# Kernel optimization log

Hardware: AMD Instinct MI355X
Metric: run time of the kernel (lower is better)

## Reference

```python
import jax, jax.numpy as jnp
import numpy as np

DIM = 768
NUM_HEADS = 8
SCALE = (DIM // NUM_HEADS) ** -0.5  # 96^-0.5, matches head_dim**-0.5
B, N = 8, 4096


def setup_inputs() -> dict:
    key = jax.random.key(0)
    k1, k2 = jax.random.split(key)
    x_1 = jax.random.normal(k1, (B, N, DIM), dtype=jnp.float32)
    x_2 = jax.random.normal(k2, (B, N, DIM), dtype=jnp.float32)
    return {"x_1": x_1, "x_2": x_2}


def reference(x_1, x_2):
    # q = x_1, k = v = x_2; channel-wise (transpose) attention
    # attn[b,c,d] = sum_n q[b,n,c] * k[b,n,d] * scale   -> [B, C, C]
    attn = jnp.einsum('bnc,bnd->bcd', x_1, x_2) * SCALE
    attn = jax.nn.softmax(attn, axis=-1)
    # out[b,c,n] = sum_d attn[b,c,d] * v[b,n,d]          -> [B, C, N]
    return jnp.einsum('bcd,bnd->bcn', attn, x_2)
```

## Files before the change

### kernel.cpp

```cpp
#include <hip/hip_runtime.h>
#include <stdint.h>

typedef _Float16 f16;
typedef _Float16 f16x4 __attribute__((ext_vector_type(4)));
typedef _Float16 f16x8 __attribute__((ext_vector_type(8)));
typedef float f32x4 __attribute__((ext_vector_type(4)));

#define NB 8
#define NN 4096
#define CC 768
#define SCALE_F 0.10206207261596577f

#define GLDS16(gp, lp)                                                       \
  __builtin_amdgcn_global_load_lds(                                          \
      (__attribute__((address_space(1))) void*)(gp),                         \
      (__attribute__((address_space(3))) void*)(lp), 16, 0, 0)

__global__ __launch_bounds__(256) void k_convert(
    const float* __restrict__ x1, const float* __restrict__ x2,
    f16* __restrict__ x1t, f16* __restrict__ x2t, f16* __restrict__ x2b) {
  __shared__ float tile[64][65];
  const int which = blockIdx.z >> 3;
  const int b = blockIdx.z & 7;
  const int n0 = blockIdx.x << 6;
  const int c0 = blockIdx.y << 6;
  const float* src = (which ? x2 : x1) + (size_t)b * NN * CC;
  f16* dt = (which ? x2t : x1t) + (size_t)b * CC * NN;
  const int t = threadIdx.x;
  const int rowi = t >> 4;
  const int col4 = (t & 15) << 2;
#pragma unroll
  for (int it = 0; it < 4; ++it) {
    const int r = it * 16 + rowi;
    const float4 v =
        *reinterpret_cast<const float4*>(&src[(size_t)(n0 + r) * CC + c0 + col4]);
    tile[r][col4 + 0] = v.x;
    tile[r][col4 + 1] = v.y;
    tile[r][col4 + 2] = v.z;
    tile[r][col4 + 3] = v.w;
    if (which) {
      f16x4 o = {(f16)v.x, (f16)v.y, (f16)v.z, (f16)v.w};
      *reinterpret_cast<f16x4*>(
          &x2b[(size_t)b * NN * CC + (size_t)(n0 + r) * CC + c0 + col4]) = o;
    }
  }
  __syncthreads();
  const int c = t >> 2;
  const int nb = (t & 3) << 4;
  f16x8 lo, hi;
#pragma unroll
  for (int j = 0; j < 8; ++j) lo[j] = (f16)tile[nb + j][c];
#pragma unroll
  for (int j = 0; j < 8; ++j) hi[j] = (f16)tile[nb + 8 + j][c];
  f16* o = &dt[(size_t)(c0 + c) * NN + n0 + nb];
  *reinterpret_cast<f16x8*>(o) = lo;
  *reinterpret_cast<f16x8*>(o + 8) = hi;
}

template <bool ATOMIC, int SWZ>
__global__ __launch_bounds__(256) void k_gemm_bt(
    const f16* __restrict__ A, const f16* __restrict__ B,
    float* __restrict__ C, int klen, int lda, int ldb, int ldc,
    size_t sA, size_t sB, size_t sC) {
  __shared__ __align__(16) f16 As[128 * 32];
  __shared__ __align__(16) f16 Bs[128 * 32];

  const int lin = blockIdx.x;
  const int xcd = lin & 7;
  const int slot = lin >> 3;
  int bx, by, b, ks;
  if (SWZ == 1) {
    b = xcd;
    ks = slot / 36;
    const int item = slot % 36;
    bx = item % 6;
    by = item / 6;
  } else {
    b = xcd;
    ks = 0;
    bx = slot / 6;
    by = slot % 6;
  }

  const f16* Ap = A + (size_t)b * sA + (size_t)by * 128 * lda + (size_t)ks * klen;
  const f16* Bp = B + (size_t)b * sB + (size_t)bx * 128 * ldb + (size_t)ks * klen;
  float* Cp = C + (size_t)b * sC + (size_t)by * 128 * ldc + bx * 128;

  const int tid = threadIdx.x;
  const int wave = tid >> 6;
  const int lane = tid & 63;
  const int wr = wave >> 1;
  const int wc = wave & 1;

  const f16* ga0 = Ap + (size_t)(wave * 32 + (lane >> 2)) * lda + (lane & 3) * 8;
  const f16* ga1 = ga0 + (size_t)16 * lda;
  const f16* gb0 = Bp + (size_t)(wave * 32 + (lane >> 2)) * ldb + (lane & 3) * 8;
  const f16* gb1 = gb0 + (size_t)16 * ldb;
  f16* la0 = As + wave * 32 * 32;
  f16* la1 = la0 + 16 * 32;
  f16* lb0 = Bs + wave * 32 * 32;
  f16* lb1 = lb0 + 16 * 32;

  const f16* ra = As + (wr * 64 + (lane & 15)) * 32 + (lane >> 4) * 8;
  const f16* rb = Bs + (wc * 64 + (lane & 15)) * 32 + (lane >> 4) * 8;

  f32x4 acc[4][4] = {};

  for (int k = 0; k < klen; k += 32) {
    __syncthreads();
    GLDS16(ga0, la0);
    GLDS16(ga1, la1);
    GLDS16(gb0, lb0);
    GLDS16(gb1, lb1);
    ga0 += 32; ga1 += 32; gb0 += 32; gb1 += 32;
    __syncthreads();
    f16x8 af[4], bfv[4];
#pragma unroll
    for (int i = 0; i < 4; ++i)
      af[i] = *reinterpret_cast<const f16x8*>(ra + i * 16 * 32);
#pragma unroll
    for (int j = 0; j < 4; ++j)
      bfv[j] = *reinterpret_cast<const f16x8*>(rb + j * 16 * 32);
#pragma unroll
    for (int i = 0; i < 4; ++i)
#pragma unroll
      for (int j = 0; j < 4; ++j)
        acc[i][j] = __builtin_amdgcn_mfma_f32_16x16x32_f16(af[i], bfv[j],
                                                           acc[i][j], 0, 0, 0);
  }

  const int col = lane & 15;
  const int rq = (lane >> 4) * 4;
#pragma unroll
  for (int i = 0; i < 4; ++i) {
    const int r0 = wr * 64 + i * 16 + rq;
#pragma unroll
    for (int j = 0; j < 4; ++j) {
      const int cidx = wc * 64 + j * 16 + col;
#pragma unroll
      for (int r = 0; r < 4; ++r) {
        const float v = acc[i][j][r];
        if (ATOMIC)
          atomicAdd(&Cp[(size_t)(r0 + r) * ldc + cidx], v);
        else
          Cp[(size_t)(r0 + r) * ldc + cidx] = v;
      }
    }
  }
}

__global__ __launch_bounds__(256) void k_softmax(const float* __restrict__ S,
                                                 f16* __restrict__ P) {
  const int row = blockIdx.x * 4 + (threadIdx.x >> 6);
  const int lane = threadIdx.x & 63;
  const float* s = S + (size_t)row * CC;
  float v[12];
#pragma unroll
  for (int j = 0; j < 3; ++j) {
    const float4 t = *reinterpret_cast<const float4*>(&s[j * 256 + lane * 4]);
    v[j * 4 + 0] = t.x * SCALE_F;
    v[j * 4 + 1] = t.y * SCALE_F;
    v[j * 4 + 2] = t.z * SCALE_F;
    v[j * 4 + 3] = t.w * SCALE_F;
  }
  float m = v[0];
#pragma unroll
  for (int j = 1; j < 12; ++j) m = fmaxf(m, v[j]);
#pragma unroll
  for (int off = 32; off >= 1; off >>= 1) m = fmaxf(m, __shfl_xor(m, off, 64));
  float sum = 0.f;
#pragma unroll
  for (int j = 0; j < 12; ++j) {
    v[j] = __expf(v[j] - m);
    sum += v[j];
  }
#pragma unroll
  for (int off = 32; off >= 1; off >>= 1) sum += __shfl_xor(sum, off, 64);
  const float inv = 1.0f / sum;
  f16* p = P + (size_t)row * CC;
#pragma unroll
  for (int j = 0; j < 3; ++j) {
    f16x4 o = {(f16)(v[j * 4 + 0] * inv), (f16)(v[j * 4 + 1] * inv),
               (f16)(v[j * 4 + 2] * inv), (f16)(v[j * 4 + 3] * inv)};
    *reinterpret_cast<f16x4*>(&p[j * 256 + lane * 4]) = o;
  }
}

extern "C" void kernel_launch(void* const* d_in, const int* in_sizes, int n_in,
                              void* d_out, int out_size, void* d_ws,
                              size_t ws_size, hipStream_t stream) {
  const float* x1 = (const float*)d_in[0];
  const float* x2 = (const float*)d_in[1];
  float* out = (float*)d_out;

  const size_t elems = (size_t)NB * NN * CC;
  f16* x1t = (f16*)d_out;
  f16* x2t = x1t + elems;
  char* ws = (char*)d_ws;
  f16* x2b = (f16*)ws;
  float* S = (float*)(ws + elems * 2);
  f16* P = (f16*)(ws + elems * 2 + (size_t)NB * CC * CC * 4);
  const size_t need =
      elems * 2 + (size_t)NB * CC * CC * 4 + (size_t)NB * CC * CC * 2;
  if (ws_size < need) return;

  k_convert<<<dim3(NN / 64, CC / 64, 2 * NB), 256, 0, stream>>>(x1, x2, x1t,
                                                                x2t, x2b);
  hipMemsetAsync(S, 0, (size_t)NB * CC * CC * 4, stream);
  k_gemm_bt<true, 1><<<dim3(6 * 6 * NB * 4), 256, 0, stream>>>(
      x1t, x2t, S, NN / 4, NN, NN, CC, (size_t)CC * NN, (size_t)CC * NN,
      (size_t)CC * CC);
  k_softmax<<<dim3(NB * CC / 4), 256, 0, stream>>>(S, P);
  k_gemm_bt<false, 2><<<dim3(32 * 6 * NB), 256, 0, stream>>>(
      P, x2b, out, CC, CC, CC, NN, (size_t)CC * CC, (size_t)NN * CC,
      (size_t)CC * NN);
}
```

Before: 428.3 us.

## Double-buffer LDS tiles in GEMM to overlap global loads with MFMA

Both GEMM kernels now use two LDS buffers for the A and B tiles. The first tile is prefetched before the loop, and each iteration issues the direct global-to-LDS loads for the next k-slice before running MFMAs on the current one. This also drops one barrier per iteration, so the global load latency can hide behind compute instead of sitting idle between two syncs. LDS use doubles, which could lower occupancy, and correctness depends on the barrier waiting for the outstanding loads into the current buffer.

```diff
diff --git a/kernel.cpp b/kernel.cpp
--- a/kernel.cpp
+++ b/kernel.cpp
@@ -62,8 +62,8 @@
     const f16* __restrict__ A, const f16* __restrict__ B,
     float* __restrict__ C, int klen, int lda, int ldb, int ldc,
     size_t sA, size_t sB, size_t sC) {
-  __shared__ __align__(16) f16 As[128 * 32];
-  __shared__ __align__(16) f16 Bs[128 * 32];
+  __shared__ __align__(16) f16 As[2][128 * 32];
+  __shared__ __align__(16) f16 Bs[2][128 * 32];
 
   const int lin = blockIdx.x;
   const int xcd = lin & 7;
@@ -96,24 +96,33 @@
   const f16* ga1 = ga0 + (size_t)16 * lda;
   const f16* gb0 = Bp + (size_t)(wave * 32 + (lane >> 2)) * ldb + (lane & 3) * 8;
   const f16* gb1 = gb0 + (size_t)16 * ldb;
-  f16* la0 = As + wave * 32 * 32;
-  f16* la1 = la0 + 16 * 32;
-  f16* lb0 = Bs + wave * 32 * 32;
-  f16* lb1 = lb0 + 16 * 32;
-
-  const f16* ra = As + (wr * 64 + (lane & 15)) * 32 + (lane >> 4) * 8;
-  const f16* rb = Bs + (wc * 64 + (lane & 15)) * 32 + (lane >> 4) * 8;
+  const int lofs0 = wave * 32 * 32;
+  const int lofs1 = lofs0 + 16 * 32;
+
+  const int raofs = (wr * 64 + (lane & 15)) * 32 + (lane >> 4) * 8;
+  const int rbofs = (wc * 64 + (lane & 15)) * 32 + (lane >> 4) * 8;
 
   f32x4 acc[4][4] = {};
 
-  for (int k = 0; k < klen; k += 32) {
+  const int nit = klen >> 5;
+  GLDS16(ga0, &As[0][lofs0]);
+  GLDS16(ga1, &As[0][lofs1]);
+  GLDS16(gb0, &Bs[0][lofs0]);
+  GLDS16(gb1, &Bs[0][lofs1]);
+
+  for (int it = 0; it < nit; ++it) {
+    const int cur = it & 1;
+    const int nxt = cur ^ 1;
     __syncthreads();
-    GLDS16(ga0, la0);
-    GLDS16(ga1, la1);
-    GLDS16(gb0, lb0);
-    GLDS16(gb1, lb1);
-    ga0 += 32; ga1 += 32; gb0 += 32; gb1 += 32;
-    __syncthreads();
+    if (it + 1 < nit) {
+      ga0 += 32; ga1 += 32; gb0 += 32; gb1 += 32;
+      GLDS16(ga0, &As[nxt][lofs0]);
+      GLDS16(ga1, &As[nxt][lofs1]);
+      GLDS16(gb0, &Bs[nxt][lofs0]);
+      GLDS16(gb1, &Bs[nxt][lofs1]);
+    }
+    const f16* ra = &As[cur][raofs];
+    const f16* rb = &Bs[cur][rbofs];
     f16x8 af[4], bfv[4];
 #pragma unroll
     for (int i = 0; i < 4; ++i)
```

After: 424.3 us. Within noise of the previous version (-0.9%).
